# Kernel tuning notes

Measured on AMD Instinct MI355X. Metric: run time of the kernel, lower is better.

Reference implementation:

```python
import jax, jax.numpy as jnp
import numpy as np

NUM_NODE = 2_000_000
DIM = 64
B, N, MAX_NB = 512, 50, 20
ALPHA = 0.2  # LeakyReLU negative slope


def setup_inputs() -> dict:
    key = jax.random.key(0)
    ks = jax.random.split(key, 11)
    stdv = 1.0 / np.sqrt(DIM)
    u = lambda k, shape: jax.random.uniform(k, shape, jnp.float32, -stdv, stdv)
    return {
        "inputs": jax.random.randint(ks[0], (B, N), 0, NUM_NODE),
        "neighbor_seqs": jax.random.randint(ks[1], (B, N, MAX_NB), 0, NUM_NODE),
        "neighbor_masks": jax.random.randint(ks[2], (B, N, MAX_NB), 0, 2).astype(jnp.int32),
        "embedding": u(ks[3], (NUM_NODE, DIM)),
        "W_ih": u(ks[4], (3 * DIM, 2 * DIM)),
        "W_hh": u(ks[5], (3 * DIM, DIM)),
        "b_ih": u(ks[6], (3 * DIM,)),
        "b_hh": u(ks[7], (3 * DIM,)),
        "attn_w1": u(ks[8], (DIM, 2 * DIM)),
        "attn_b1": u(ks[9], (DIM,)),
        "attn_w2": u(ks[10], (1, DIM)),
    }


def _gru(x, W_ih, W_hh, b_ih, b_hh):
    """PyTorch-semantics GRU, batch_first. x: (S, T, 2D) -> out: (S, T, D)."""
    D = W_hh.shape[1]
    gx = jnp.einsum('std,gd->stg', x, W_ih) + b_ih  # (S, T, 3D) input gates

    def step(h, gx_t):
        gh = h @ W_hh.T + b_hh
        rx, zx, nx = jnp.split(gx_t, 3, axis=-1)
        rh, zh, nh = jnp.split(gh, 3, axis=-1)
        r = jax.nn.sigmoid(rx + rh)
        z = jax.nn.sigmoid(zx + zh)
        n = jnp.tanh(nx + r * nh)
        h_new = (1.0 - z) * n + z * h
        return h_new, h_new

    h0 = jnp.zeros((x.shape[0], D), x.dtype)
    _, ys = jax.lax.scan(step, h0, jnp.swapaxes(gx, 0, 1))  # (T, S, D)
    return jnp.swapaxes(ys, 0, 1)


def reference(inputs, neighbor_seqs, neighbor_masks, embedding,
              W_ih, W_hh, b_ih, b_hh, attn_w1, attn_b1, attn_w2):
    # h = normalize(E[inputs])  (B, N, D)
    h = embedding[inputs]
    h = h / jnp.clip(jnp.linalg.norm(h, axis=-1, keepdims=True), 1e-12)
    nb = embedding[neighbor_seqs]  # (B, N, T, D) irregular gather
    Bn, Nn, T, D = nb.shape

    central = jnp.broadcast_to(h[:, :, None, :], nb.shape)  # (B, N, T, D)
    gru_in = jnp.concatenate([nb, central], axis=-1).reshape(Bn * Nn, T, 2 * D)
    gru_out = _gru(gru_in, W_ih, W_hh, b_ih, b_hh).reshape(Bn, Nn, T, D)

    # attention scores over neighbors
    a_in = jnp.concatenate([gru_out, central], axis=-1)  # (B, N, T, 2D)
    hid = jax.nn.leaky_relu(jnp.einsum('bntd,kd->bntk', a_in, attn_w1) + attn_b1, ALPHA)
    scores = jnp.einsum('bntk,k->bnt', hid, attn_w2[0])
    scores = jnp.where(neighbor_masks == 0, -1e9, scores)
    beta = jax.nn.softmax(scores, axis=-1)

    z_fast = jnp.einsum('bnt,bntd->bnd', beta, nb)
    has_nb = (neighbor_masks.sum(axis=-1, keepdims=True) > 0).astype(h.dtype)
    return z_fast * has_nb + h * (1.0 - has_nb)
```

## Files before the change

### kernel.cpp

```cpp
#include <hip/hip_runtime.h>
#include <cstddef>

#define TTT   20
#define SBLK  16
#define GRIDN 1600
#define BLOCK 256

typedef __attribute__((ext_vector_type(8))) _Float16 f16x8;
typedef __attribute__((ext_vector_type(4))) _Float16 f16x4;
typedef __attribute__((ext_vector_type(4))) float    f32x4;

struct BF { f16x8 hi, lo; };

__device__ __forceinline__ BF load_bf(const float* rowp, int lane) {
  BF fr;
  const float* p = rowp + ((lane >> 4) << 3);
  float t[8];
  *(float4*)&t[0] = *(const float4*)(p);
  *(float4*)&t[4] = *(const float4*)(p + 4);
#pragma unroll
  for (int jj = 0; jj < 8; ++jj) {
    const _Float16 h = (_Float16)t[jj];
    fr.hi[jj] = h;
    fr.lo[jj] = (_Float16)(t[jj] - (float)h);
  }
  return fr;
}

__device__ __forceinline__ f32x4 mfma3(f16x8 ah, f16x8 al, const BF& b, f32x4 c) {
  c = __builtin_amdgcn_mfma_f32_16x16x32_f16(ah, b.hi, c, 0, 0, 0);
  c = __builtin_amdgcn_mfma_f32_16x16x32_f16(ah, b.lo, c, 0, 0, 0);
  c = __builtin_amdgcn_mfma_f32_16x16x32_f16(al, b.hi, c, 0, 0, 0);
  return c;
}

__global__ void __launch_bounds__(BLOCK, 2) gat_gru_v2(
    const int*   __restrict__ g_inputs,
    const int*   __restrict__ g_nseq,
    const int*   __restrict__ g_nmask,
    const float* __restrict__ g_emb,
    const float* __restrict__ g_wih,
    const float* __restrict__ g_whh,
    const float* __restrict__ g_bih,
    const float* __restrict__ g_bhh,
    const float* __restrict__ g_aw1,
    const float* __restrict__ g_ab1,
    const float* __restrict__ g_aw2,
    float*       __restrict__ g_out)
{
  __shared__ _Float16 AFhi[2][2048];
  __shared__ _Float16 AFlo[2][2048];
  __shared__ float    SCP[TTT * 4 * 16];
  __shared__ float    SC2[16 * TTT];
  __shared__ float    BB [16 * TTT];
  __shared__ float    HN [16 * 64];
  __shared__ int      HAS[16];

  const int tid  = threadIdx.x;
  const int lane = tid & 63;
  const int w    = tid >> 6;
  const int s    = tid >> 4;
  const int j    = tid & 15;
  const int g    = lane >> 4;
  const int f    = w * 16 + (lane & 15);
  const int sbase = blockIdx.x * SBLK;
  const size_t snb = (size_t)(sbase + s) * TTT;

  const int ci = g_inputs[sbase + s];
  const float4 cent0 = *(const float4*)(g_emb + (size_t)ci * 64 + j * 4);
  const int idx0 = g_nseq[snb];
  const float4 nb0 = *(const float4*)(g_emb + (size_t)idx0 * 64 + j * 4);

  const float w2f  = g_aw2[f];
  const float bihr = g_bih[f], bihz = g_bih[64 + f], bihn = g_bih[128 + f];
  const float bhhr = g_bhh[f], bhhz = g_bhh[64 + f], bhhn = g_bhh[128 + f];
  const float ab1f = g_ab1[f];

  BF B0r[2], B0z[2], B0nx[2], B0at[2];
#pragma unroll
  for (int k2 = 0; k2 < 2; ++k2) {
    B0r[k2]  = load_bf(g_wih + (size_t)f * 128         + 64 + k2 * 32, lane);
    B0z[k2]  = load_bf(g_wih + (size_t)(64 + f) * 128  + 64 + k2 * 32, lane);
    B0nx[k2] = load_bf(g_wih + (size_t)(128 + f) * 128 + 64 + k2 * 32, lane);
    B0at[k2] = load_bf(g_aw1 + (size_t)f * 128         + 64 + k2 * 32, lane);
  }

  float hv4[4] = {cent0.x, cent0.y, cent0.z, cent0.w};
  {
    float ssum = hv4[0]*hv4[0] + hv4[1]*hv4[1] + hv4[2]*hv4[2] + hv4[3]*hv4[3];
    ssum += __shfl_xor(ssum, 1, 64); ssum += __shfl_xor(ssum, 2, 64);
    ssum += __shfl_xor(ssum, 4, 64); ssum += __shfl_xor(ssum, 8, 64);
    const float inv = 1.f / fmaxf(sqrtf(ssum), 1e-12f);
#pragma unroll
    for (int c = 0; c < 4; ++c) hv4[c] *= inv;
    *(float4*)&HN[s * 64 + j * 4] = *(float4*)hv4;
    const int k0 = 4 * j;
    const int e  = ((k0 >> 3) * 16 + s) * 8 + (k0 & 7);
    f16x4 hi, lo;
#pragma unroll
    for (int c = 0; c < 4; ++c) {
      hi[c] = (_Float16)hv4[c];
      lo[c] = (_Float16)(hv4[c] - (float)hi[c]);
    }
    *(f16x4*)&AFhi[0][e] = hi;
    *(f16x4*)&AFlo[0][e] = lo;
  }
  __syncthreads();

  f32x4 cr, cz, cnh, cnx, cat;
  {
    f32x4 a_r, a_z, a_nx, a_at;
#pragma unroll
    for (int q = 0; q < 4; ++q) { a_r[q] = 0.f; a_z[q] = 0.f; a_nx[q] = 0.f; a_at[q] = 0.f; }
#pragma unroll
    for (int k2 = 0; k2 < 2; ++k2) {
      const f16x8 ah = *(const f16x8*)&AFhi[0][k2 * 512 + lane * 8];
      const f16x8 al = *(const f16x8*)&AFlo[0][k2 * 512 + lane * 8];
      a_r  = mfma3(ah, al, B0r[k2],  a_r);
      a_z  = mfma3(ah, al, B0z[k2],  a_z);
      a_nx = mfma3(ah, al, B0nx[k2], a_nx);
      a_at = mfma3(ah, al, B0at[k2], a_at);
    }
#pragma unroll
    for (int q = 0; q < 4; ++q) {
      cr[q]  = a_r[q]  + bihr + bhhr;
      cz[q]  = a_z[q]  + bihz + bhhz;
      cnh[q] = bhhn;
      cnx[q] = a_nx[q] + bihn;
      cat[q] = a_at[q] + ab1f;
    }
  }

  {
    const int k0 = 4 * j;
    const int e  = ((k0 >> 3) * 16 + s) * 8 + (k0 & 7);
    f16x4 z4;
#pragma unroll
    for (int c = 0; c < 4; ++c) z4[c] = (_Float16)0.f;
    *(f16x4*)&AFhi[1][e] = z4;
    *(f16x4*)&AFlo[1][e] = z4;
    const int k1 = 64 + 4 * j;
    const int e1 = ((k1 >> 3) * 16 + s) * 8 + (k1 & 7);
    float tv[4] = {nb0.x, nb0.y, nb0.z, nb0.w};
    f16x4 hi, lo;
#pragma unroll
    for (int c = 0; c < 4; ++c) {
      hi[c] = (_Float16)tv[c];
      lo[c] = (_Float16)(tv[c] - (float)hi[c]);
    }
    *(f16x4*)&AFhi[1][e1] = hi;
    *(f16x4*)&AFlo[1][e1] = lo;
  }

  BF Br[4], Bz[4], Bnh[2], Bnx[2], Bat[2];
#pragma unroll
  for (int k2 = 0; k2 < 2; ++k2) {
    Br[k2]     = load_bf(g_whh + (size_t)f * 64          + k2 * 32, lane);
    Br[2 + k2] = load_bf(g_wih + (size_t)f * 128         + k2 * 32, lane);
    Bz[k2]     = load_bf(g_whh + (size_t)(64 + f) * 64   + k2 * 32, lane);
    Bz[2 + k2] = load_bf(g_wih + (size_t)(64 + f) * 128  + k2 * 32, lane);
    Bnh[k2]    = load_bf(g_whh + (size_t)(128 + f) * 64  + k2 * 32, lane);
    Bnx[k2]    = load_bf(g_wih + (size_t)(128 + f) * 128 + k2 * 32, lane);
    Bat[k2]    = load_bf(g_aw1 + (size_t)f * 128         + k2 * 32, lane);
  }
  float hp[4] = {0.f, 0.f, 0.f, 0.f};
  __syncthreads();

  for (int it = 0; it <= TTT; ++it) {
    const int rd  = (it + 1) & 1;
    const int wrb = it & 1;
    const bool full = (it < TTT);
    const bool dog  = (it < TTT - 1);
    float4 nb4;
    if (dog) {
      const int idx = g_nseq[snb + it + 1];
      nb4 = *(const float4*)(g_emb + (size_t)idx * 64 + j * 4);
    }

    f32x4 ar = cr, az = cz, anh = cnh, anx = cnx, aat = cat;
#pragma unroll
    for (int k2 = 0; k2 < 2; ++k2) {
      const f16x8 ah = *(const f16x8*)&AFhi[rd][k2 * 512 + lane * 8];
      const f16x8 al = *(const f16x8*)&AFlo[rd][k2 * 512 + lane * 8];
      aat = mfma3(ah, al, Bat[k2], aat);
      if (full) {
        ar  = mfma3(ah, al, Br[k2],  ar);
        az  = mfma3(ah, al, Bz[k2],  az);
        anh = mfma3(ah, al, Bnh[k2], anh);
      }
    }
    if (full) {
#pragma unroll
      for (int k2 = 0; k2 < 2; ++k2) {
        const f16x8 ah = *(const f16x8*)&AFhi[rd][(2 + k2) * 512 + lane * 8];
        const f16x8 al = *(const f16x8*)&AFlo[rd][(2 + k2) * 512 + lane * 8];
        ar  = mfma3(ah, al, Br[2 + k2], ar);
        az  = mfma3(ah, al, Bz[2 + k2], az);
        anx = mfma3(ah, al, Bnx[k2],    anx);
      }
    }

    if (it >= 1) {
      float c0, c1, c2, c3;
      {
        float a;
        a = aat[0]; c0 = w2f * (a > 0.f ? a : 0.2f * a);
        a = aat[1]; c1 = w2f * (a > 0.f ? a : 0.2f * a);
        a = aat[2]; c2 = w2f * (a > 0.f ? a : 0.2f * a);
        a = aat[3]; c3 = w2f * (a > 0.f ? a : 0.2f * a);
      }
#pragma unroll
      for (int m = 1; m < 16; m <<= 1) {
        c0 += __shfl_xor(c0, m, 64); c1 += __shfl_xor(c1, m, 64);
        c2 += __shfl_xor(c2, m, 64); c3 += __shfl_xor(c3, m, 64);
      }
      if ((lane & 15) == 0) {
        float4 pv; pv.x = c0; pv.y = c1; pv.z = c2; pv.w = c3;
        *(float4*)&SCP[((it - 1) * 4 + w) * 16 + g * 4] = pv;
      }
    }

    if (full) {
      const int kc = f >> 3, fb = f & 7;
#pragma unroll
      for (int q = 0; q < 4; ++q) {
        const float r  = 1.f / (1.f + __expf(-ar[q]));
        const float zz = 1.f / (1.f + __expf(-az[q]));
        const float u  = __expf(2.f * (anx[q] + r * anh[q]));
        const float n  = 1.f - 2.f / (u + 1.f);
        const float hnew = (1.f - zz) * n + zz * hp[q];
        hp[q] = hnew;
        const _Float16 hh = (_Float16)hnew;
        const int e = (kc * 16 + g * 4 + q) * 8 + fb;
        AFhi[wrb][e] = hh;
        AFlo[wrb][e] = (_Float16)(hnew - (float)hh);
      }
      if (dog) {
        const int k1 = 64 + 4 * j;
        const int e1 = ((k1 >> 3) * 16 + s) * 8 + (k1 & 7);
        float tv[4] = {nb4.x, nb4.y, nb4.z, nb4.w};
        f16x4 hi, lo;
#pragma unroll
        for (int c = 0; c < 4; ++c) {
          hi[c] = (_Float16)tv[c];
          lo[c] = (_Float16)(tv[c] - (float)hi[c]);
        }
        *(f16x4*)&AFhi[wrb][e1] = hi;
        *(f16x4*)&AFlo[wrb][e1] = lo;
      }
    }
    __syncthreads();
  }

  {
    const int s1 = tid & 15, t0 = tid >> 4;
#pragma unroll
    for (int rep = 0; rep < 2; ++rep) {
      const int t = t0 + rep * 16;
      if (t < TTT) {
        const float sc = SCP[t * 64 + s1] + SCP[t * 64 + 16 + s1] +
                         SCP[t * 64 + 32 + s1] + SCP[t * 64 + 48 + s1];
        const int mk = g_nmask[(size_t)(sbase + s1) * TTT + t];
        SC2[s1 * TTT + t] = mk ? sc : -1e30f;
      }
    }
  }
  __syncthreads();
  {
    const float v0 = SC2[s * TTT + j];
    const float v1 = (j < 4) ? SC2[s * TTT + 16 + j] : -1e30f;
    float mx = fmaxf(v0, v1);
#pragma unroll
    for (int m = 1; m < 16; m <<= 1) mx = fmaxf(mx, __shfl_xor(mx, m, 64));
    const float e0 = (v0 > -1e29f) ? __expf(v0 - mx) : 0.f;
    const float e1 = (v1 > -1e29f) ? __expf(v1 - mx) : 0.f;
    float sm = e0 + e1;
#pragma unroll
    for (int m = 1; m < 16; m <<= 1) sm += __shfl_xor(sm, m, 64);
    const float rinv = (sm > 0.f) ? 1.f / sm : 0.f;
    BB[s * TTT + j] = e0 * rinv;
    if (j < 4) BB[s * TTT + 16 + j] = e1 * rinv;
    if (j == 0) HAS[s] = (sm > 0.f) ? 1 : 0;
  }
  __syncthreads();
  {
    float za[4] = {0.f, 0.f, 0.f, 0.f};
    for (int t = 0; t < TTT; ++t) {
      const float b = BB[s * TTT + t];
      if (b != 0.f) {
        const int idx = g_nseq[snb + t];
        const float4 e4 = *(const float4*)(g_emb + (size_t)idx * 64 + j * 4);
        za[0] += b * e4.x; za[1] += b * e4.y; za[2] += b * e4.z; za[3] += b * e4.w;
      }
    }
    float4 o;
    if (HAS[s]) { o.x = za[0]; o.y = za[1]; o.z = za[2]; o.w = za[3]; }
    else        { o = *(float4*)&HN[s * 64 + j * 4]; }
    *(float4*)(g_out + (size_t)(sbase + s) * 64 + j * 4) = o;
  }
}

extern "C" void kernel_launch(void* const* d_in, const int* in_sizes, int n_in,
                              void* d_out, int out_size, void* d_ws, size_t ws_size,
                              hipStream_t stream) {
  (void)in_sizes; (void)n_in; (void)out_size; (void)d_ws; (void)ws_size;
  gat_gru_v2<<<GRIDN, BLOCK, 0, stream>>>(
      (const int*)d_in[0], (const int*)d_in[1], (const int*)d_in[2],
      (const float*)d_in[3], (const float*)d_in[4], (const float*)d_in[5],
      (const float*)d_in[6], (const float*)d_in[7], (const float*)d_in[8],
      (const float*)d_in[9], (const float*)d_in[10],
      (float*)d_out);
}
```

Before: 733.0 us.

## Give each wave its own 16 sequences with shared LDS weights and no block barriers

Restructures the fused GRU+attention kernel so each wave handles 16 sequences across all 64 hidden features, instead of four waves splitting features over one 16-sequence group. The split-fp16 weight fragments are staged once per block in a large dynamic LDS buffer. Per-wave state tiles remove the per-timestep __syncthreads and the cross-wave score reduction, and the softmax and weighted sum run per wave from register state. The cost is 150KB of LDS, which limits occupancy to one block per CU, many more LDS reads of weights per step, and higher register pressure from the 4x accumulator tiles.

```diff
diff --git a/kernel.cpp b/kernel.cpp
--- a/kernel.cpp
+++ b/kernel.cpp
@@ -2,9 +2,9 @@
 #include <cstddef>
 
 #define TTT   20
-#define SBLK  16
-#define GRIDN 1600
+#define GRIDN 400
 #define BLOCK 256
+#define LDSB  152576
 
 typedef __attribute__((ext_vector_type(8))) _Float16 f16x8;
 typedef __attribute__((ext_vector_type(4))) _Float16 f16x4;
@@ -27,14 +27,14 @@
   return fr;
 }
 
-__device__ __forceinline__ f32x4 mfma3(f16x8 ah, f16x8 al, const BF& b, f32x4 c) {
-  c = __builtin_amdgcn_mfma_f32_16x16x32_f16(ah, b.hi, c, 0, 0, 0);
-  c = __builtin_amdgcn_mfma_f32_16x16x32_f16(ah, b.lo, c, 0, 0, 0);
-  c = __builtin_amdgcn_mfma_f32_16x16x32_f16(al, b.hi, c, 0, 0, 0);
+__device__ __forceinline__ f32x4 mfma3w(f16x8 wh, f16x8 wl, f16x8 sh, f16x8 sl, f32x4 c) {
+  c = __builtin_amdgcn_mfma_f32_16x16x32_f16(wh, sh, c, 0, 0, 0);
+  c = __builtin_amdgcn_mfma_f32_16x16x32_f16(wl, sh, c, 0, 0, 0);
+  c = __builtin_amdgcn_mfma_f32_16x16x32_f16(wh, sl, c, 0, 0, 0);
   return c;
 }
 
-__global__ void __launch_bounds__(BLOCK, 2) gat_gru_v2(
+__global__ void __launch_bounds__(BLOCK, 1) gat_gru_v5(
     const int*   __restrict__ g_inputs,
     const int*   __restrict__ g_nseq,
     const int*   __restrict__ g_nmask,
@@ -48,255 +48,316 @@
     const float* __restrict__ g_aw2,
     float*       __restrict__ g_out)
 {
-  __shared__ _Float16 AFhi[2][2048];
-  __shared__ _Float16 AFlo[2][2048];
-  __shared__ float    SCP[TTT * 4 * 16];
-  __shared__ float    SC2[16 * TTT];
-  __shared__ float    BB [16 * TTT];
-  __shared__ float    HN [16 * 64];
-  __shared__ int      HAS[16];
+  extern __shared__ char smem[];
+  _Float16* WF = (_Float16*)smem;
+  _Float16* ST = WF + 56 * 1024;
+  float*    SCb = (float*)(smem + 147456);
 
   const int tid  = threadIdx.x;
   const int lane = tid & 63;
   const int w    = tid >> 6;
-  const int s    = tid >> 4;
-  const int j    = tid & 15;
+  const int l15  = lane & 15;
   const int g    = lane >> 4;
-  const int f    = w * 16 + (lane & 15);
-  const int sbase = blockIdx.x * SBLK;
-  const size_t snb = (size_t)(sbase + s) * TTT;
-
-  const int ci = g_inputs[sbase + s];
-  const float4 cent0 = *(const float4*)(g_emb + (size_t)ci * 64 + j * 4);
-  const int idx0 = g_nseq[snb];
-  const float4 nb0 = *(const float4*)(g_emb + (size_t)idx0 * 64 + j * 4);
-
-  const float w2f  = g_aw2[f];
-  const float bihr = g_bih[f], bihz = g_bih[64 + f], bihn = g_bih[128 + f];
-  const float bhhr = g_bhh[f], bhhz = g_bhh[64 + f], bhhn = g_bhh[128 + f];
-  const float ab1f = g_ab1[f];
-
-  BF B0r[2], B0z[2], B0nx[2], B0at[2];
+  const int seqq = lane >> 2;
+  const int part = lane & 3;
+  const int gseq0 = blockIdx.x * 64 + w * 16;
+  const int gseq  = gseq0 + seqq;
+
+  _Float16* SThi = ST + w * 4096;
+  _Float16* STlo = SThi + 2048;
+  float*    SCw  = SCb + w * 320;
+
+  for (int u = tid; u < 3584; u += BLOCK) {
+    const int fid  = u >> 6;
+    const int slot = u & 63;
+    const int sl15 = slot & 15, sg = slot >> 4;
+    int kt, gi, tile;
+    if (fid < 32) { kt = fid >> 4; gi = (fid >> 2) & 3; tile = fid & 3; }
+    else { const int r2 = fid - 32; kt = 2 + (r2 >= 12); gi = (r2 % 12) >> 2; tile = r2 & 3; }
+    const int f = tile * 16 + sl15;
+    const float* src;
+    if (kt < 2) {
+      const int kc = kt * 32 + sg * 8;
+      if (gi == 0)      src = g_whh + (size_t)f * 64 + kc;
+      else if (gi == 1) src = g_whh + (size_t)(64 + f) * 64 + kc;
+      else if (gi == 2) src = g_whh + (size_t)(128 + f) * 64 + kc;
+      else              src = g_aw1 + (size_t)f * 128 + kc;
+    } else {
+      const int kc = (kt - 2) * 32 + sg * 8;
+      if (gi == 0)      src = g_wih + (size_t)f * 128 + kc;
+      else if (gi == 1) src = g_wih + (size_t)(64 + f) * 128 + kc;
+      else              src = g_wih + (size_t)(128 + f) * 128 + kc;
+    }
+    float t8[8];
+    *(float4*)&t8[0] = *(const float4*)(src);
+    *(float4*)&t8[4] = *(const float4*)(src + 4);
+    f16x8 hi, lo;
+#pragma unroll
+    for (int jj = 0; jj < 8; ++jj) {
+      const _Float16 h = (_Float16)t8[jj];
+      hi[jj] = h; lo[jj] = (_Float16)(t8[jj] - (float)h);
+    }
+    *(f16x8*)&WF[fid * 1024 + slot * 8]       = hi;
+    *(f16x8*)&WF[fid * 1024 + 512 + slot * 8] = lo;
+  }
+
+  f32x4 cva[4];
+  {
+    const int ci = g_inputs[gseq];
+    const float* cp = g_emb + (size_t)ci * 64 + part * 16;
+#pragma unroll
+    for (int i = 0; i < 4; ++i) cva[i] = *(const f32x4*)(cp + i * 4);
+    float ss = 0.f;
+#pragma unroll
+    for (int i = 0; i < 4; ++i)
+#pragma unroll
+      for (int q = 0; q < 4; ++q) ss += cva[i][q] * cva[i][q];
+    ss += __shfl_xor(ss, 1, 64); ss += __shfl_xor(ss, 2, 64);
+    const float inv = 1.f / fmaxf(sqrtf(ss), 1e-12f);
+#pragma unroll
+    for (int i = 0; i < 4; ++i) {
+      f16x4 h4, l4;
+#pragma unroll
+      for (int q = 0; q < 4; ++q) {
+        const float v = cva[i][q] * inv;
+        const _Float16 hh = (_Float16)v;
+        h4[q] = hh; l4[q] = (_Float16)(v - (float)hh);
+      }
+      const int e = ((part * 2 + (i >> 1)) * 16 + seqq) * 8 + (i & 1) * 4;
+      *(f16x4*)&SThi[e] = h4;
+      *(f16x4*)&STlo[e] = l4;
+    }
+  }
+  asm volatile("" ::: "memory");
+
+  f32x4 cr[4], cz[4], cnh[4], cnx[4], cat[4], w24[4];
+#pragma unroll
+  for (int t = 0; t < 4; ++t)
+#pragma unroll
+    for (int q = 0; q < 4; ++q) { cr[t][q]=0.f; cz[t][q]=0.f; cnx[t][q]=0.f; cat[t][q]=0.f; }
 #pragma unroll
   for (int k2 = 0; k2 < 2; ++k2) {
-    B0r[k2]  = load_bf(g_wih + (size_t)f * 128         + 64 + k2 * 32, lane);
-    B0z[k2]  = load_bf(g_wih + (size_t)(64 + f) * 128  + 64 + k2 * 32, lane);
-    B0nx[k2] = load_bf(g_wih + (size_t)(128 + f) * 128 + 64 + k2 * 32, lane);
-    B0at[k2] = load_bf(g_aw1 + (size_t)f * 128         + 64 + k2 * 32, lane);
-  }
-
-  float hv4[4] = {cent0.x, cent0.y, cent0.z, cent0.w};
+    const f16x8 sh = *(const f16x8*)&SThi[k2 * 512 + lane * 8];
+    const f16x8 sl = *(const f16x8*)&STlo[k2 * 512 + lane * 8];
+#pragma unroll
+    for (int t = 0; t < 4; ++t) {
+      BF b;
+      b = load_bf(g_wih + (size_t)(t*16 + l15) * 128 + 64 + k2*32, lane);
+      cr[t]  = mfma3w(b.hi, b.lo, sh, sl, cr[t]);
+      b = load_bf(g_wih + (size_t)(64 + t*16 + l15) * 128 + 64 + k2*32, lane);
+      cz[t]  = mfma3w(b.hi, b.lo, sh, sl, cz[t]);
+      b = load_bf(g_wih + (size_t)(128 + t*16 + l15) * 128 + 64 + k2*32, lane);
+      cnx[t] = mfma3w(b.hi, b.lo, sh, sl, cnx[t]);
+      b = load_bf(g_aw1 + (size_t)(t*16 + l15) * 128 + 64 + k2*32, lane);
+      cat[t] = mfma3w(b.hi, b.lo, sh, sl, cat[t]);
+    }
+  }
+#pragma unroll
+  for (int t = 0; t < 4; ++t) {
+    const int f0 = t * 16 + g * 4;
+    const f32x4 br1 = *(const f32x4*)(g_bih + f0),       br2 = *(const f32x4*)(g_bhh + f0);
+    const f32x4 bz1 = *(const f32x4*)(g_bih + 64 + f0),  bz2 = *(const f32x4*)(g_bhh + 64 + f0);
+    cnh[t] = *(const f32x4*)(g_bhh + 128 + f0);
+    const f32x4 bn1 = *(const f32x4*)(g_bih + 128 + f0);
+    const f32x4 ba  = *(const f32x4*)(g_ab1 + f0);
+    w24[t] = *(const f32x4*)(g_aw2 + f0);
+#pragma unroll
+    for (int q = 0; q < 4; ++q) {
+      cr[t][q] += br1[q] + br2[q];
+      cz[t][q] += bz1[q] + bz2[q];
+      cnx[t][q] += bn1[q];
+      cat[t][q] += ba[q];
+    }
+  }
+  asm volatile("" ::: "memory");
+
   {
-    float ssum = hv4[0]*hv4[0] + hv4[1]*hv4[1] + hv4[2]*hv4[2] + hv4[3]*hv4[3];
-    ssum += __shfl_xor(ssum, 1, 64); ssum += __shfl_xor(ssum, 2, 64);
-    ssum += __shfl_xor(ssum, 4, 64); ssum += __shfl_xor(ssum, 8, 64);
-    const float inv = 1.f / fmaxf(sqrtf(ssum), 1e-12f);
-#pragma unroll
-    for (int c = 0; c < 4; ++c) hv4[c] *= inv;
-    *(float4*)&HN[s * 64 + j * 4] = *(float4*)hv4;
-    const int k0 = 4 * j;
-    const int e  = ((k0 >> 3) * 16 + s) * 8 + (k0 & 7);
-    f16x4 hi, lo;
-#pragma unroll
-    for (int c = 0; c < 4; ++c) {
-      hi[c] = (_Float16)hv4[c];
-      lo[c] = (_Float16)(hv4[c] - (float)hi[c]);
-    }
-    *(f16x4*)&AFhi[0][e] = hi;
-    *(f16x4*)&AFlo[0][e] = lo;
-  }
+    const int idx0 = g_nseq[(size_t)gseq * TTT];
+    const float* rp = g_emb + (size_t)idx0 * 64 + part * 16;
+#pragma unroll
+    for (int i = 0; i < 4; ++i) {
+      const f32x4 v4 = *(const f32x4*)(rp + i * 4);
+      f16x4 h4, l4;
+#pragma unroll
+      for (int q = 0; q < 4; ++q) {
+        const _Float16 hh = (_Float16)v4[q];
+        h4[q] = hh; l4[q] = (_Float16)(v4[q] - (float)hh);
+      }
+      const int e = ((8 + part * 2 + (i >> 1)) * 16 + seqq) * 8 + (i & 1) * 4;
+      *(f16x4*)&SThi[e] = h4;
+      *(f16x4*)&STlo[e] = l4;
+    }
+  }
+  f32x4 hp[4];
+#pragma unroll
+  for (int t = 0; t < 4; ++t)
+#pragma unroll
+    for (int q = 0; q < 4; ++q) hp[t][q] = 0.f;
+
   __syncthreads();
 
-  f32x4 cr, cz, cnh, cnx, cat;
-  {
-    f32x4 a_r, a_z, a_nx, a_at;
-#pragma unroll
-    for (int q = 0; q < 4; ++q) { a_r[q] = 0.f; a_z[q] = 0.f; a_nx[q] = 0.f; a_at[q] = 0.f; }
-#pragma unroll
-    for (int k2 = 0; k2 < 2; ++k2) {
-      const f16x8 ah = *(const f16x8*)&AFhi[0][k2 * 512 + lane * 8];
-      const f16x8 al = *(const f16x8*)&AFlo[0][k2 * 512 + lane * 8];
-      a_r  = mfma3(ah, al, B0r[k2],  a_r);
-      a_z  = mfma3(ah, al, B0z[k2],  a_z);
-      a_nx = mfma3(ah, al, B0nx[k2], a_nx);
-      a_at = mfma3(ah, al, B0at[k2], a_at);
-    }
-#pragma unroll
-    for (int q = 0; q < 4; ++q) {
-      cr[q]  = a_r[q]  + bihr + bhhr;
-      cz[q]  = a_z[q]  + bihz + bhhz;
-      cnh[q] = bhhn;
-      cnx[q] = a_nx[q] + bihn;
-      cat[q] = a_at[q] + ab1f;
-    }
-  }
-
-  {
-    const int k0 = 4 * j;
-    const int e  = ((k0 >> 3) * 16 + s) * 8 + (k0 & 7);
-    f16x4 z4;
-#pragma unroll
-    for (int c = 0; c < 4; ++c) z4[c] = (_Float16)0.f;
-    *(f16x4*)&AFhi[1][e] = z4;
-    *(f16x4*)&AFlo[1][e] = z4;
-    const int k1 = 64 + 4 * j;
-    const int e1 = ((k1 >> 3) * 16 + s) * 8 + (k1 & 7);
-    float tv[4] = {nb0.x, nb0.y, nb0.z, nb0.w};
-    f16x4 hi, lo;
-#pragma unroll
-    for (int c = 0; c < 4; ++c) {
-      hi[c] = (_Float16)tv[c];
-      lo[c] = (_Float16)(tv[c] - (float)hi[c]);
-    }
-    *(f16x4*)&AFhi[1][e1] = hi;
-    *(f16x4*)&AFlo[1][e1] = lo;
-  }
-
-  BF Br[4], Bz[4], Bnh[2], Bnx[2], Bat[2];
-#pragma unroll
-  for (int k2 = 0; k2 < 2; ++k2) {
-    Br[k2]     = load_bf(g_whh + (size_t)f * 64          + k2 * 32, lane);
-    Br[2 + k2] = load_bf(g_wih + (size_t)f * 128         + k2 * 32, lane);
-    Bz[k2]     = load_bf(g_whh + (size_t)(64 + f) * 64   + k2 * 32, lane);
-    Bz[2 + k2] = load_bf(g_wih + (size_t)(64 + f) * 128  + k2 * 32, lane);
-    Bnh[k2]    = load_bf(g_whh + (size_t)(128 + f) * 64  + k2 * 32, lane);
-    Bnx[k2]    = load_bf(g_wih + (size_t)(128 + f) * 128 + k2 * 32, lane);
-    Bat[k2]    = load_bf(g_aw1 + (size_t)f * 128         + k2 * 32, lane);
-  }
-  float hp[4] = {0.f, 0.f, 0.f, 0.f};
-  __syncthreads();
-
+  auto ldw = [&](int fid, f16x8& wh, f16x8& wl) {
+    wh = *(const f16x8*)&WF[fid * 1024 + lane * 8];
+    wl = *(const f16x8*)&WF[fid * 1024 + 512 + lane * 8];
+  };
+
+#pragma unroll 1
   for (int it = 0; it <= TTT; ++it) {
-    const int rd  = (it + 1) & 1;
-    const int wrb = it & 1;
     const bool full = (it < TTT);
     const bool dog  = (it < TTT - 1);
-    float4 nb4;
+    f32x4 nbv[4];
     if (dog) {
-      const int idx = g_nseq[snb + it + 1];
-      nb4 = *(const float4*)(g_emb + (size_t)idx * 64 + j * 4);
-    }
-
-    f32x4 ar = cr, az = cz, anh = cnh, anx = cnx, aat = cat;
-#pragma unroll
-    for (int k2 = 0; k2 < 2; ++k2) {
-      const f16x8 ah = *(const f16x8*)&AFhi[rd][k2 * 512 + lane * 8];
-      const f16x8 al = *(const f16x8*)&AFlo[rd][k2 * 512 + lane * 8];
-      aat = mfma3(ah, al, Bat[k2], aat);
-      if (full) {
-        ar  = mfma3(ah, al, Br[k2],  ar);
-        az  = mfma3(ah, al, Bz[k2],  az);
-        anh = mfma3(ah, al, Bnh[k2], anh);
+      const int idx = g_nseq[(size_t)gseq * TTT + it + 1];
+      const float* rp = g_emb + (size_t)idx * 64 + part * 16;
+#pragma unroll
+      for (int i = 0; i < 4; ++i) nbv[i] = *(const f32x4*)(rp + i * 4);
+    }
+    f32x4 ar[4], az[4], anh[4], anx[4], aat[4];
+#pragma unroll
+    for (int t = 0; t < 4; ++t) {
+      aat[t] = cat[t];
+      if (full) { ar[t]=cr[t]; az[t]=cz[t]; anh[t]=cnh[t]; anx[t]=cnx[t]; }
+    }
+    if (it >= 1) {
+#pragma unroll
+      for (int k2 = 0; k2 < 2; ++k2) {
+        const f16x8 sh = *(const f16x8*)&SThi[k2 * 512 + lane * 8];
+        const f16x8 sl = *(const f16x8*)&STlo[k2 * 512 + lane * 8];
+#pragma unroll
+        for (int t = 0; t < 4; ++t) {
+          f16x8 wh, wl;
+          ldw(k2*16 + 12 + t, wh, wl); aat[t] = mfma3w(wh, wl, sh, sl, aat[t]);
+          if (full) {
+            ldw(k2*16 + t,     wh, wl); ar[t]  = mfma3w(wh, wl, sh, sl, ar[t]);
+            ldw(k2*16 + 4 + t, wh, wl); az[t]  = mfma3w(wh, wl, sh, sl, az[t]);
+            ldw(k2*16 + 8 + t, wh, wl); anh[t] = mfma3w(wh, wl, sh, sl, anh[t]);
+          }
+        }
       }
     }
     if (full) {
 #pragma unroll
       for (int k2 = 0; k2 < 2; ++k2) {
-        const f16x8 ah = *(const f16x8*)&AFhi[rd][(2 + k2) * 512 + lane * 8];
-        const f16x8 al = *(const f16x8*)&AFlo[rd][(2 + k2) * 512 + lane * 8];
-        ar  = mfma3(ah, al, Br[2 + k2], ar);
-        az  = mfma3(ah, al, Bz[2 + k2], az);
-        anx = mfma3(ah, al, Bnx[k2],    anx);
-      }
-    }
+        const f16x8 sh = *(const f16x8*)&SThi[(2 + k2) * 512 + lane * 8];
+        const f16x8 sl = *(const f16x8*)&STlo[(2 + k2) * 512 + lane * 8];
+#pragma unroll
+        for (int t = 0; t < 4; ++t) {
+          f16x8 wh, wl;
+          ldw(32 + k2*12 + t,     wh, wl); ar[t]  = mfma3w(wh, wl, sh, sl, ar[t]);
+          ldw(32 + k2*12 + 4 + t, wh, wl); az[t]  = mfma3w(wh, wl, sh, sl, az[t]);
+          ldw(32 + k2*12 + 8 + t, wh, wl); anx[t] = mfma3w(wh, wl, sh, sl, anx[t]);
+        }
+      }
+    }
+    asm volatile("" ::: "memory");
 
     if (it >= 1) {
-      float c0, c1, c2, c3;
-      {
-        float a;
-        a = aat[0]; c0 = w2f * (a > 0.f ? a : 0.2f * a);
-        a = aat[1]; c1 = w2f * (a > 0.f ? a : 0.2f * a);
-        a = aat[2]; c2 = w2f * (a > 0.f ? a : 0.2f * a);
-        a = aat[3]; c3 = w2f * (a > 0.f ? a : 0.2f * a);
-      }
-#pragma unroll
-      for (int m = 1; m < 16; m <<= 1) {
-        c0 += __shfl_xor(c0, m, 64); c1 += __shfl_xor(c1, m, 64);
-        c2 += __shfl_xor(c2, m, 64); c3 += __shfl_xor(c3, m, 64);
-      }
-      if ((lane & 15) == 0) {
-        float4 pv; pv.x = c0; pv.y = c1; pv.z = c2; pv.w = c3;
-        *(float4*)&SCP[((it - 1) * 4 + w) * 16 + g * 4] = pv;
-      }
-    }
-
+      float p = 0.f;
+#pragma unroll
+      for (int t = 0; t < 4; ++t)
+#pragma unroll
+        for (int q = 0; q < 4; ++q) {
+          const float a = aat[t][q];
+          p += w24[t][q] * (a > 0.f ? a : 0.2f * a);
+        }
+      p += __shfl_xor(p, 16, 64);
+      p += __shfl_xor(p, 32, 64);
+      if (g == 0) SCw[l15 * TTT + (it - 1)] = p;
+    }
     if (full) {
-      const int kc = f >> 3, fb = f & 7;
-#pragma unroll
-      for (int q = 0; q < 4; ++q) {
-        const float r  = 1.f / (1.f + __expf(-ar[q]));
-        const float zz = 1.f / (1.f + __expf(-az[q]));
-        const float u  = __expf(2.f * (anx[q] + r * anh[q]));
-        const float n  = 1.f - 2.f / (u + 1.f);
-        const float hnew = (1.f - zz) * n + zz * hp[q];
-        hp[q] = hnew;
-        const _Float16 hh = (_Float16)hnew;
-        const int e = (kc * 16 + g * 4 + q) * 8 + fb;
-        AFhi[wrb][e] = hh;
-        AFlo[wrb][e] = (_Float16)(hnew - (float)hh);
+#pragma unroll
+      for (int t = 0; t < 4; ++t) {
+        f16x4 h4, l4;
+#pragma unroll
+        for (int q = 0; q < 4; ++q) {
+          const float r  = 1.f / (1.f + __expf(-ar[t][q]));
+          const float zz = 1.f / (1.f + __expf(-az[t][q]));
+          const float u  = __expf(2.f * (anx[t][q] + r * anh[t][q]));
+          const float n  = 1.f - 2.f / (u + 1.f);
+          const float hnew = (1.f - zz) * n + zz * hp[t][q];
+          hp[t][q] = hnew;
+          const _Float16 hh = (_Float16)hnew;
+          h4[q] = hh; l4[q] = (_Float16)(hnew - (float)hh);
+        }
+        const int eh = ((t * 2 + (g >> 1)) * 16 + l15) * 8 + (g & 1) * 4;
+        *(f16x4*)&SThi[eh] = h4;
+        *(f16x4*)&STlo[eh] = l4;
       }
       if (dog) {
-        const int k1 = 64 + 4 * j;
-        const int e1 = ((k1 >> 3) * 16 + s) * 8 + (k1 & 7);
-        float tv[4] = {nb4.x, nb4.y, nb4.z, nb4.w};
-        f16x4 hi, lo;
-#pragma unroll
-        for (int c = 0; c < 4; ++c) {
-          hi[c] = (_Float16)tv[c];
-          lo[c] = (_Float16)(tv[c] - (float)hi[c]);
-        }
-        *(f16x4*)&AFhi[wrb][e1] = hi;
-        *(f16x4*)&AFlo[wrb][e1] = lo;
-      }
-    }
-    __syncthreads();
+#pragma unroll
+        for (int i = 0; i < 4; ++i) {
+          f16x4 h4, l4;
+#pragma unroll
+          for (int q = 0; q < 4; ++q) {
+            const _Float16 hh = (_Float16)nbv[i][q];
+            h4[q] = hh; l4[q] = (_Float16)(nbv[i][q] - (float)hh);
+          }
+          const int e = ((8 + part * 2 + (i >> 1)) * 16 + seqq) * 8 + (i & 1) * 4;
+          *(f16x4*)&SThi[e] = h4;
+          *(f16x4*)&STlo[e] = l4;
+        }
+      }
+    }
+    asm volatile("" ::: "memory");
   }
 
   {
-    const int s1 = tid & 15, t0 = tid >> 4;
-#pragma unroll
-    for (int rep = 0; rep < 2; ++rep) {
-      const int t = t0 + rep * 16;
-      if (t < TTT) {
-        const float sc = SCP[t * 64 + s1] + SCP[t * 64 + 16 + s1] +
-                         SCP[t * 64 + 32 + s1] + SCP[t * 64 + 48 + s1];
-        const int mk = g_nmask[(size_t)(sbase + s1) * TTT + t];
-        SC2[s1 * TTT + t] = mk ? sc : -1e30f;
-      }
-    }
-  }
-  __syncthreads();
-  {
-    const float v0 = SC2[s * TTT + j];
-    const float v1 = (j < 4) ? SC2[s * TTT + 16 + j] : -1e30f;
-    float mx = fmaxf(v0, v1);
-#pragma unroll
-    for (int m = 1; m < 16; m <<= 1) mx = fmaxf(mx, __shfl_xor(mx, m, 64));
-    const float e0 = (v0 > -1e29f) ? __expf(v0 - mx) : 0.f;
-    const float e1 = (v1 > -1e29f) ? __expf(v1 - mx) : 0.f;
-    float sm = e0 + e1;
-#pragma unroll
-    for (int m = 1; m < 16; m <<= 1) sm += __shfl_xor(sm, m, 64);
-    const float rinv = (sm > 0.f) ? 1.f / sm : 0.f;
-    BB[s * TTT + j] = e0 * rinv;
-    if (j < 4) BB[s * TTT + 16 + j] = e1 * rinv;
-    if (j == 0) HAS[s] = (sm > 0.f) ? 1 : 0;
-  }
-  __syncthreads();
-  {
-    float za[4] = {0.f, 0.f, 0.f, 0.f};
+    int mbits = 0;
+    float mx = -1e30f;
+#pragma unroll
     for (int t = 0; t < TTT; ++t) {
-      const float b = BB[s * TTT + t];
-      if (b != 0.f) {
-        const int idx = g_nseq[snb + t];
-        const float4 e4 = *(const float4*)(g_emb + (size_t)idx * 64 + j * 4);
-        za[0] += b * e4.x; za[1] += b * e4.y; za[2] += b * e4.z; za[3] += b * e4.w;
-      }
-    }
-    float4 o;
-    if (HAS[s]) { o.x = za[0]; o.y = za[1]; o.z = za[2]; o.w = za[3]; }
-    else        { o = *(float4*)&HN[s * 64 + j * 4]; }
-    *(float4*)(g_out + (size_t)(sbase + s) * 64 + j * 4) = o;
+      if (g_nmask[(size_t)gseq * TTT + t]) {
+        mbits |= (1 << t);
+        mx = fmaxf(mx, SCw[seqq * TTT + t]);
+      }
+    }
+    float sum = 0.f;
+    f32x4 za[4];
+#pragma unroll
+    for (int i = 0; i < 4; ++i)
+#pragma unroll
+      for (int q = 0; q < 4; ++q) za[i][q] = 0.f;
+    for (int t = 0; t < TTT; ++t) {
+      if (mbits & (1 << t)) {
+        const float e = __expf(SCw[seqq * TTT + t] - mx);
+        sum += e;
+        const int idx = g_nseq[(size_t)gseq * TTT + t];
+        const float* rp = g_emb + (size_t)idx * 64 + part * 16;
+#pragma unroll
+        for (int i = 0; i < 4; ++i) {
+          const f32x4 e4 = *(const f32x4*)(rp + i * 4);
+#pragma unroll
+          for (int q = 0; q < 4; ++q) za[i][q] += e * e4[q];
+        }
+      }
+    }
+    f32x4 o[4];
+    if (mbits) {
+      const float inv = 1.f / sum;
+#pragma unroll
+      for (int i = 0; i < 4; ++i)
+#pragma unroll
+        for (int q = 0; q < 4; ++q) o[i][q] = za[i][q] * inv;
+    } else {
+      const int ci = g_inputs[gseq];
+      const float* cp = g_emb + (size_t)ci * 64 + part * 16;
+      float ss = 0.f;
+#pragma unroll
+      for (int i = 0; i < 4; ++i) {
+        o[i] = *(const f32x4*)(cp + i * 4);
+#pragma unroll
+        for (int q = 0; q < 4; ++q) ss += o[i][q] * o[i][q];
+      }
+      ss += __shfl_xor(ss, 1, 64); ss += __shfl_xor(ss, 2, 64);
+      const float inv = 1.f / fmaxf(sqrtf(ss), 1e-12f);
+#pragma unroll
+      for (int i = 0; i < 4; ++i)
+#pragma unroll
+        for (int q = 0; q < 4; ++q) o[i][q] *= inv;
+    }
+    float* op = g_out + (size_t)gseq * 64 + part * 16;
+#pragma unroll
+    for (int i = 0; i < 4; ++i) *(f32x4*)(op + i * 4) = o[i];
   }
 }
 
@@ -304,7 +365,9 @@
                               void* d_out, int out_size, void* d_ws, size_t ws_size,
                               hipStream_t stream) {
   (void)in_sizes; (void)n_in; (void)out_size; (void)d_ws; (void)ws_size;
-  gat_gru_v2<<<GRIDN, BLOCK, 0, stream>>>(
+  (void)hipFuncSetAttribute((const void*)gat_gru_v5,
+                            hipFuncAttributeMaxDynamicSharedMemorySize, LDSB);
+  gat_gru_v5<<<GRIDN, BLOCK, LDSB, stream>>>(
       (const int*)d_in[0], (const int*)d_in[1], (const int*)d_in[2],
       (const float*)d_in[3], (const float*)d_in[4], (const float*)d_in[5],
       (const float*)d_in[6], (const float*)d_in[7], (const float*)d_in[8],
```

After: 924.8 us. 26.2% more time.
